# Performance work log

Measured on AMD Instinct MI355X. Metric: run time of the kernel, lower is better.

The kernel has to match this reference:

```python
import jax, jax.numpy as jnp
import numpy as np

# J2 (von Mises) plane-strain elastoplasticity with linear isotropic hardening
# (faithful stand-in for pyprnn's J2Material: elastic predictor + radial return,
#  committed history = plastic strain tensor + accumulated plastic strain).
E_MOD = 3130.0   # Young's modulus (epoxy, MPa)
NU = 0.37        # Poisson ratio
SIG_Y = 64.8     # initial yield stress
H_ISO = 300.0    # linear isotropic hardening modulus
MU = E_MOD / (2.0 * (1.0 + NU))
LAM = E_MOD * NU / ((1.0 + NU) * (1.0 - 2.0 * NU))


def j2_update(eps, eps_p, alpha):
    """eps: [P,3] (exx, eyy, gamma_xy engineering); eps_p: [P,4] (xx,yy,zz,xy tensorial);
    alpha: [P] accumulated plastic strain. Returns (stress [P,3], eps_p_new, alpha_new)."""
    ee_xx = eps[:, 0] - eps_p[:, 0]
    ee_yy = eps[:, 1] - eps_p[:, 1]
    ee_zz = -eps_p[:, 2]                      # plane strain: total ezz = 0
    ee_xy = 0.5 * eps[:, 2] - eps_p[:, 3]     # tensorial shear
    tr = ee_xx + ee_yy + ee_zz
    # trial (elastic predictor) stress
    sxx = LAM * tr + 2.0 * MU * ee_xx
    syy = LAM * tr + 2.0 * MU * ee_yy
    szz = LAM * tr + 2.0 * MU * ee_zz
    sxy = 2.0 * MU * ee_xy
    p = (sxx + syy + szz) / 3.0
    dxx, dyy, dzz = sxx - p, syy - p, szz - p
    q = jnp.sqrt(1.5 * (dxx * dxx + dyy * dyy + dzz * dzz + 2.0 * sxy * sxy))
    f = q - (SIG_Y + H_ISO * alpha)
    dgam = jnp.maximum(f, 0.0) / (3.0 * MU + H_ISO)   # radial return, closed form
    qs = jnp.maximum(q, 1e-12)
    nxx, nyy, nzz, nxy = 1.5 * dxx / qs, 1.5 * dyy / qs, 1.5 * dzz / qs, 1.5 * sxy / qs
    two_mu_dg = 2.0 * MU * dgam
    sig = jnp.stack([sxx - two_mu_dg * nxx, syy - two_mu_dg * nyy, sxy - two_mu_dg * nxy], axis=-1)
    eps_p_new = eps_p + dgam[:, None] * jnp.stack([nxx, nyy, nzz, nxy], axis=-1)
    alpha_new = alpha + dgam
    return sig, eps_p_new, alpha_new


def setup_inputs() -> dict:
    key = jax.random.key(0)
    k1, k2, k3 = jax.random.split(key, 3)
    B, T, F = 16384, 128, 3
    MATPTS = 16
    L, O = MATPTS * F, 3
    x = jax.random.normal(k1, (B, T, F), dtype=jnp.float32) * 0.02  # strain paths
    W1 = jax.random.normal(k2, (L, F), dtype=jnp.float32) * (1.0 / np.sqrt(F))
    W2 = jax.random.normal(k3, (O, L), dtype=jnp.float32) * (1.0 / np.sqrt(L))
    return {"x": x, "W1": W1, "W2": W2}


def reference(x, W1, W2):
    B, T, F = x.shape
    L = W1.shape[0]
    P = B * (L // F)                 # total material points = batch * mat_pts
    W2s = jax.nn.softplus(W2)        # SoftLayer: positive weights, no bias
    xt = jnp.swapaxes(x, 0, 1)       # [T, B, F]

    def step(carry, xi):
        eps_p, alpha = carry
        lat = xi @ W1.T                       # fc1 (no bias): [B, L]
        eps = lat.reshape(P, F)               # per-material-point strain
        sig, eps_p, alpha = j2_update(eps, eps_p, alpha)   # update + commit
        out = sig.reshape(B, L) @ W2s.T       # fc2 softplus-weighted linear
        return (eps_p, alpha), out

    carry0 = (jnp.zeros((P, 4), jnp.float32), jnp.zeros((P,), jnp.float32))
    _, ys = jax.lax.scan(step, carry0, xt)    # ys: [T, B, O]
    return jnp.swapaxes(ys, 0, 1)             # [B, T, O]
```

## Files before the change

### kernel.cpp

```cpp
#include <hip/hip_runtime.h>
#include <math.h>


#define BLOCK 256
#define BPB 16
#define TSTEPS 128
#define ROWF (TSTEPS * 3)
#define ROWP 388

#define DPP_REDUCE3(a, b, c)                                                          \
  asm volatile(                                                                       \
    "s_nop 1\n\t"                                                                     \
    "v_add_f32_dpp %0, %0, %0 row_shr:1 row_mask:0xf bank_mask:0xf bound_ctrl:1\n\t"  \
    "v_add_f32_dpp %1, %1, %1 row_shr:1 row_mask:0xf bank_mask:0xf bound_ctrl:1\n\t"  \
    "v_add_f32_dpp %2, %2, %2 row_shr:1 row_mask:0xf bank_mask:0xf bound_ctrl:1\n\t"  \
    "v_add_f32_dpp %0, %0, %0 row_shr:2 row_mask:0xf bank_mask:0xf bound_ctrl:1\n\t"  \
    "v_add_f32_dpp %1, %1, %1 row_shr:2 row_mask:0xf bank_mask:0xf bound_ctrl:1\n\t"  \
    "v_add_f32_dpp %2, %2, %2 row_shr:2 row_mask:0xf bank_mask:0xf bound_ctrl:1\n\t"  \
    "v_add_f32_dpp %0, %0, %0 row_shr:4 row_mask:0xf bank_mask:0xf bound_ctrl:1\n\t"  \
    "v_add_f32_dpp %1, %1, %1 row_shr:4 row_mask:0xf bank_mask:0xf bound_ctrl:1\n\t"  \
    "v_add_f32_dpp %2, %2, %2 row_shr:4 row_mask:0xf bank_mask:0xf bound_ctrl:1\n\t"  \
    "v_add_f32_dpp %0, %0, %0 row_shr:8 row_mask:0xf bank_mask:0xf bound_ctrl:1\n\t"  \
    "v_add_f32_dpp %1, %1, %1 row_shr:8 row_mask:0xf bank_mask:0xf bound_ctrl:1\n\t"  \
    "v_add_f32_dpp %2, %2, %2 row_shr:8 row_mask:0xf bank_mask:0xf bound_ctrl:1"      \
    : "+v"(a), "+v"(b), "+v"(c))

__global__ __launch_bounds__(BLOCK, 4)
void prnn_j2_kernel(const float* __restrict__ x,
                    const float* __restrict__ W1,
                    const float* __restrict__ W2,
                    float* __restrict__ out)
{
    constexpr float MU    = (float)(3130.0 / (2.0 * (1.0 + 0.37)));
    constexpr float LAM   = (float)(3130.0 * 0.37 / ((1.0 + 0.37) * (1.0 - 2.0 * 0.37)));
    constexpr float SIG_Y = 64.8f;
    constexpr float H_ISO = 300.0f;
    const float TWO_MU  = 2.0f * MU;
    const float K3MU    = 3.0f * MU;
    const float INV_DEN = 1.0f / (3.0f * MU + H_ISO);
    const float KBULK   = LAM + TWO_MU * (1.0f / 3.0f);
    const float C_Q2    = 6.0f * MU * MU;

    __shared__ float xs[BPB * ROWP + 12];

    const int tid = threadIdx.x;
    const int bl  = tid >> 4;
    const int m   = tid & 15;
    const bool m15 = (m == 15);
    const int blockBase = blockIdx.x * (BPB * ROWF);

    for (int i = tid; i < BPB * ROWF; i += BLOCK) {
        int b = i / ROWF;
        int r = i - b * ROWF;
        xs[b * ROWP + r] = x[blockBase + i];
    }

    float w1[3][3], w2s[3][3];
    #pragma unroll
    for (int c = 0; c < 3; ++c)
        #pragma unroll
        for (int f = 0; f < 3; ++f)
            w1[c][f] = W1[(3 * m + c) * 3 + f];
    #pragma unroll
    for (int o = 0; o < 3; ++o)
        #pragma unroll
        for (int c = 0; c < 3; ++c) {
            float w = W2[o * 48 + 3 * m + c];
            w2s[o][c] = fmaxf(w, 0.0f) + log1pf(expf(-fabsf(w)));
        }

    __syncthreads();

    float p0 = 0.f, p1 = 0.f, p2 = 0.f, p3 = 0.f;
    float yld = SIG_Y;
    float* xrow = &xs[bl * ROWP];
    float4* xv  = (float4*)xrow;

#define J2_STEP(x0_, x1_, x2_, wp_)                                          \
  {                                                                          \
    const float x0 = (x0_), x1 = (x1_), x2 = (x2_);                          \
    const float e0 = w1[0][0]*x0 + w1[0][1]*x1 + w1[0][2]*x2;                \
    const float e1 = w1[1][0]*x0 + w1[1][1]*x1 + w1[1][2]*x2;                \
    const float e2 = w1[2][0]*x0 + w1[2][1]*x1 + w1[2][2]*x2;                \
    const float ee_xx = e0 - p0;                                             \
    const float ee_yy = e1 - p1;                                             \
    const float ee_xy = fmaf(0.5f, e2, -p3);                                 \
    const float tr = (ee_xx + ee_yy) - p2;                                   \
    const float c3 = tr * (1.0f/3.0f);                                       \
    const float exd = ee_xx - c3;                                            \
    const float eyd = ee_yy - c3;                                            \
    const float ezd = -p2 - c3;                                              \
    float u = exd*exd; u = fmaf(eyd, eyd, u); u = fmaf(ezd, ezd, u);         \
    u = fmaf(ee_xy*ee_xy, 2.0f, u);                                          \
    const float q2 = fmaxf(C_Q2 * u, 1e-24f);                                \
    const float rq = __builtin_amdgcn_rsqf(q2);                              \
    const float q  = q2 * rq;                                                \
    const float dgam = fmaxf(q - yld, 0.0f) * INV_DEN;                       \
    yld = fmaf(H_ISO, dgam, yld);                                            \
    const float k   = K3MU * dgam * rq;                                      \
    const float omk = 1.0f - k;                                              \
    const float pm  = KBULK * tr;                                            \
    const float s0 = fmaf(TWO_MU*exd, omk, pm);                              \
    const float s1 = fmaf(TWO_MU*eyd, omk, pm);                              \
    const float s2 = (TWO_MU*ee_xy) * omk;                                   \
    p0 = fmaf(k, exd, p0);                                                   \
    p1 = fmaf(k, eyd, p1);                                                   \
    p2 = fmaf(k, ezd, p2);                                                   \
    p3 = fmaf(k, ee_xy, p3);                                                 \
    float o0 = w2s[0][0]*s0 + w2s[0][1]*s1 + w2s[0][2]*s2;                   \
    float o1 = w2s[1][0]*s0 + w2s[1][1]*s1 + w2s[1][2]*s2;                   \
    float o2 = w2s[2][0]*s0 + w2s[2][1]*s1 + w2s[2][2]*s2;                   \
    DPP_REDUCE3(o0, o1, o2);                                                 \
    if (m15) { (wp_)[0] = o0; (wp_)[1] = o1; (wp_)[2] = o2; }                \
  }

    float4 A = xv[0], Bv = xv[1], Cv = xv[2];
    for (int tb = 0; tb < TSTEPS / 4; ++tb) {
        float4 An = xv[3 * tb + 3];
        float4 Bn = xv[3 * tb + 4];
        float4 Cn = xv[3 * tb + 5];

        float* wp = xrow + 12 * tb;
        J2_STEP(A.x, A.y, A.z,  wp + 0);
        J2_STEP(A.w, Bv.x, Bv.y, wp + 3);
        J2_STEP(Bv.z, Bv.w, Cv.x, wp + 6);
        J2_STEP(Cv.y, Cv.z, Cv.w, wp + 9);

        A = An; Bv = Bn; Cv = Cn;
    }
#undef J2_STEP

    __syncthreads();

    for (int i = tid; i < BPB * ROWF; i += BLOCK) {
        int b = i / ROWF;
        int r = i - b * ROWF;
        out[blockBase + i] = xs[b * ROWP + r];
    }
}

extern "C" void kernel_launch(void* const* d_in, const int* in_sizes, int n_in,
                              void* d_out, int out_size, void* d_ws, size_t ws_size,
                              hipStream_t stream) {
    const float* x  = (const float*)d_in[0];
    const float* W1 = (const float*)d_in[1];
    const float* W2 = (const float*)d_in[2];
    float* out = (float*)d_out;

    const int B = 16384;
    dim3 grid(B / BPB);
    dim3 block(BLOCK);
    prnn_j2_kernel<<<grid, block, 0, stream>>>(x, W1, W2, out);
}
```

Before: 135.0 us.

## Pack two material points per thread with float2 math and 8-lane butterfly reduce

Each thread now handles two material points, using 2-wide vector types so the compiler can emit packed FP32 instructions. Each batch row then needs only 8 lanes, so a block covers 32 rows. The cross-lane sum becomes a 3-stage DPP butterfly over 8 lanes instead of a 4-stage shift reduction over 16. Global loads and stores are widened to float4. The trade-off is doubled per-thread state, shared memory and register pressure, with launch bounds lowered to 2 blocks per CU, and only 3 of every 8 lanes do the output writes.

```diff
diff --git a/kernel.cpp b/kernel.cpp
--- a/kernel.cpp
+++ b/kernel.cpp
@@ -3,29 +3,35 @@
 
 
 #define BLOCK 256
-#define BPB 16
+#define BPB 32
 #define TSTEPS 128
 #define ROWF (TSTEPS * 3)
 #define ROWP 388
 
-#define DPP_REDUCE3(a, b, c)                                                          \
-  asm volatile(                                                                       \
-    "s_nop 1\n\t"                                                                     \
-    "v_add_f32_dpp %0, %0, %0 row_shr:1 row_mask:0xf bank_mask:0xf bound_ctrl:1\n\t"  \
-    "v_add_f32_dpp %1, %1, %1 row_shr:1 row_mask:0xf bank_mask:0xf bound_ctrl:1\n\t"  \
-    "v_add_f32_dpp %2, %2, %2 row_shr:1 row_mask:0xf bank_mask:0xf bound_ctrl:1\n\t"  \
-    "v_add_f32_dpp %0, %0, %0 row_shr:2 row_mask:0xf bank_mask:0xf bound_ctrl:1\n\t"  \
-    "v_add_f32_dpp %1, %1, %1 row_shr:2 row_mask:0xf bank_mask:0xf bound_ctrl:1\n\t"  \
-    "v_add_f32_dpp %2, %2, %2 row_shr:2 row_mask:0xf bank_mask:0xf bound_ctrl:1\n\t"  \
-    "v_add_f32_dpp %0, %0, %0 row_shr:4 row_mask:0xf bank_mask:0xf bound_ctrl:1\n\t"  \
-    "v_add_f32_dpp %1, %1, %1 row_shr:4 row_mask:0xf bank_mask:0xf bound_ctrl:1\n\t"  \
-    "v_add_f32_dpp %2, %2, %2 row_shr:4 row_mask:0xf bank_mask:0xf bound_ctrl:1\n\t"  \
-    "v_add_f32_dpp %0, %0, %0 row_shr:8 row_mask:0xf bank_mask:0xf bound_ctrl:1\n\t"  \
-    "v_add_f32_dpp %1, %1, %1 row_shr:8 row_mask:0xf bank_mask:0xf bound_ctrl:1\n\t"  \
-    "v_add_f32_dpp %2, %2, %2 row_shr:8 row_mask:0xf bank_mask:0xf bound_ctrl:1"      \
+typedef float v2 __attribute__((ext_vector_type(2)));
+
+static __device__ __forceinline__ v2 vfma(v2 a, v2 b, v2 c) {
+    return __builtin_elementwise_fma(a, b, c);
+}
+static __device__ __forceinline__ v2 vmax(v2 a, v2 b) {
+    return __builtin_elementwise_max(a, b);
+}
+
+#define DPP_BFLY3(a, b, c)                                                       \
+  asm volatile(                                                                  \
+    "s_nop 1\n\t"                                                                \
+    "v_add_f32_dpp %0, %0, %0 quad_perm:[1,0,3,2] row_mask:0xf bank_mask:0xf\n\t"\
+    "v_add_f32_dpp %1, %1, %1 quad_perm:[1,0,3,2] row_mask:0xf bank_mask:0xf\n\t"\
+    "v_add_f32_dpp %2, %2, %2 quad_perm:[1,0,3,2] row_mask:0xf bank_mask:0xf\n\t"\
+    "v_add_f32_dpp %0, %0, %0 quad_perm:[2,3,0,1] row_mask:0xf bank_mask:0xf\n\t"\
+    "v_add_f32_dpp %1, %1, %1 quad_perm:[2,3,0,1] row_mask:0xf bank_mask:0xf\n\t"\
+    "v_add_f32_dpp %2, %2, %2 quad_perm:[2,3,0,1] row_mask:0xf bank_mask:0xf\n\t"\
+    "v_add_f32_dpp %0, %0, %0 row_half_mirror row_mask:0xf bank_mask:0xf\n\t"    \
+    "v_add_f32_dpp %1, %1, %1 row_half_mirror row_mask:0xf bank_mask:0xf\n\t"    \
+    "v_add_f32_dpp %2, %2, %2 row_half_mirror row_mask:0xf bank_mask:0xf"        \
     : "+v"(a), "+v"(b), "+v"(c))
 
-__global__ __launch_bounds__(BLOCK, 4)
+__global__ __launch_bounds__(BLOCK, 2)
 void prnn_j2_kernel(const float* __restrict__ x,
                     const float* __restrict__ W1,
                     const float* __restrict__ W2,
@@ -40,78 +46,97 @@
     const float INV_DEN = 1.0f / (3.0f * MU + H_ISO);
     const float KBULK   = LAM + TWO_MU * (1.0f / 3.0f);
     const float C_Q2    = 6.0f * MU * MU;
+    const v2 VTHIRD = {1.0f/3.0f, 1.0f/3.0f};
+    const v2 VQMIN  = {1e-24f, 1e-24f};
+    const v2 VZERO  = {0.0f, 0.0f};
 
     __shared__ float xs[BPB * ROWP + 12];
 
     const int tid = threadIdx.x;
-    const int bl  = tid >> 4;
-    const int m   = tid & 15;
-    const bool m15 = (m == 15);
+    const int bl  = tid >> 3;
+    const int l   = tid & 7;
     const int blockBase = blockIdx.x * (BPB * ROWF);
 
-    for (int i = tid; i < BPB * ROWF; i += BLOCK) {
-        int b = i / ROWF;
-        int r = i - b * ROWF;
-        xs[b * ROWP + r] = x[blockBase + i];
+    {
+        const float4* xg = (const float4*)(x + blockBase);
+        for (int i4 = tid; i4 < BPB * ROWF / 4; i4 += BLOCK) {
+            int b  = i4 / (ROWF / 4);
+            int r4 = i4 - b * (ROWF / 4);
+            ((float4*)(xs + b * ROWP))[r4] = xg[i4];
+        }
     }
 
-    float w1[3][3], w2s[3][3];
+    const int pa = l, pb = l + 8;
+    v2 w1p[3][3], w2p[3][3];
     #pragma unroll
     for (int c = 0; c < 3; ++c)
         #pragma unroll
-        for (int f = 0; f < 3; ++f)
-            w1[c][f] = W1[(3 * m + c) * 3 + f];
+        for (int f = 0; f < 3; ++f) {
+            w1p[c][f].x = W1[(3 * pa + c) * 3 + f];
+            w1p[c][f].y = W1[(3 * pb + c) * 3 + f];
+        }
     #pragma unroll
     for (int o = 0; o < 3; ++o)
         #pragma unroll
         for (int c = 0; c < 3; ++c) {
-            float w = W2[o * 48 + 3 * m + c];
-            w2s[o][c] = fmaxf(w, 0.0f) + log1pf(expf(-fabsf(w)));
+            float wa = W2[o * 48 + 3 * pa + c];
+            float wb = W2[o * 48 + 3 * pb + c];
+            w2p[o][c].x = fmaxf(wa, 0.0f) + log1pf(expf(-fabsf(wa)));
+            w2p[o][c].y = fmaxf(wb, 0.0f) + log1pf(expf(-fabsf(wb)));
         }
 
     __syncthreads();
 
-    float p0 = 0.f, p1 = 0.f, p2 = 0.f, p3 = 0.f;
-    float yld = SIG_Y;
+    v2 p0 = VZERO, p1 = VZERO, p2 = VZERO, p3 = VZERO;
+    v2 yld = {SIG_Y, SIG_Y};
     float* xrow = &xs[bl * ROWP];
-    float4* xv  = (float4*)xrow;
+    const float4* xv = (const float4*)xrow;
 
 #define J2_STEP(x0_, x1_, x2_, wp_)                                          \
   {                                                                          \
-    const float x0 = (x0_), x1 = (x1_), x2 = (x2_);                          \
-    const float e0 = w1[0][0]*x0 + w1[0][1]*x1 + w1[0][2]*x2;                \
-    const float e1 = w1[1][0]*x0 + w1[1][1]*x1 + w1[1][2]*x2;                \
-    const float e2 = w1[2][0]*x0 + w1[2][1]*x1 + w1[2][2]*x2;                \
-    const float ee_xx = e0 - p0;                                             \
-    const float ee_yy = e1 - p1;                                             \
-    const float ee_xy = fmaf(0.5f, e2, -p3);                                 \
-    const float tr = (ee_xx + ee_yy) - p2;                                   \
-    const float c3 = tr * (1.0f/3.0f);                                       \
-    const float exd = ee_xx - c3;                                            \
-    const float eyd = ee_yy - c3;                                            \
-    const float ezd = -p2 - c3;                                              \
-    float u = exd*exd; u = fmaf(eyd, eyd, u); u = fmaf(ezd, ezd, u);         \
-    u = fmaf(ee_xy*ee_xy, 2.0f, u);                                          \
-    const float q2 = fmaxf(C_Q2 * u, 1e-24f);                                \
-    const float rq = __builtin_amdgcn_rsqf(q2);                              \
-    const float q  = q2 * rq;                                                \
-    const float dgam = fmaxf(q - yld, 0.0f) * INV_DEN;                       \
-    yld = fmaf(H_ISO, dgam, yld);                                            \
-    const float k   = K3MU * dgam * rq;                                      \
-    const float omk = 1.0f - k;                                              \
-    const float pm  = KBULK * tr;                                            \
-    const float s0 = fmaf(TWO_MU*exd, omk, pm);                              \
-    const float s1 = fmaf(TWO_MU*eyd, omk, pm);                              \
-    const float s2 = (TWO_MU*ee_xy) * omk;                                   \
-    p0 = fmaf(k, exd, p0);                                                   \
-    p1 = fmaf(k, eyd, p1);                                                   \
-    p2 = fmaf(k, ezd, p2);                                                   \
-    p3 = fmaf(k, ee_xy, p3);                                                 \
-    float o0 = w2s[0][0]*s0 + w2s[0][1]*s1 + w2s[0][2]*s2;                   \
-    float o1 = w2s[1][0]*s0 + w2s[1][1]*s1 + w2s[1][2]*s2;                   \
-    float o2 = w2s[2][0]*s0 + w2s[2][1]*s1 + w2s[2][2]*s2;                   \
-    DPP_REDUCE3(o0, o1, o2);                                                 \
-    if (m15) { (wp_)[0] = o0; (wp_)[1] = o1; (wp_)[2] = o2; }                \
+    const float x0s = (x0_), x1s = (x1_), x2s = (x2_);                       \
+    const v2 x0 = {x0s, x0s}, x1 = {x1s, x1s}, x2 = {x2s, x2s};              \
+    const v2 e0 = vfma(w1p[0][0], x0, vfma(w1p[0][1], x1, w1p[0][2] * x2));  \
+    const v2 e1 = vfma(w1p[1][0], x0, vfma(w1p[1][1], x1, w1p[1][2] * x2));  \
+    const v2 e2 = vfma(w1p[2][0], x0, vfma(w1p[2][1], x1, w1p[2][2] * x2));  \
+    const v2 ee_xx = e0 - p0;                                                \
+    const v2 ee_yy = e1 - p1;                                                \
+    const v2 ee_xy = 0.5f * e2 - p3;                                         \
+    const v2 tr = (ee_xx + ee_yy) - p2;                                      \
+    const v2 c3 = tr * VTHIRD;                                               \
+    const v2 exd = ee_xx - c3;                                               \
+    const v2 eyd = ee_yy - c3;                                               \
+    const v2 ezd = -p2 - c3;                                                 \
+    v2 u = exd * exd;                                                        \
+    u = vfma(eyd, eyd, u);                                                   \
+    u = vfma(ezd, ezd, u);                                                   \
+    const v2 t2 = ee_xy * ee_xy;                                             \
+    u = vfma(t2, (v2){2.0f, 2.0f}, u);                                       \
+    const v2 q2 = vmax(C_Q2 * u, VQMIN);                                     \
+    v2 rq;                                                                   \
+    rq.x = __builtin_amdgcn_rsqf(q2.x);                                      \
+    rq.y = __builtin_amdgcn_rsqf(q2.y);                                      \
+    const v2 q = q2 * rq;                                                    \
+    const v2 dgam = vmax(q - yld, VZERO) * INV_DEN;                          \
+    yld = vfma((v2){H_ISO, H_ISO}, dgam, yld);                               \
+    const v2 k   = (K3MU * dgam) * rq;                                       \
+    const v2 omk = 1.0f - k;                                                 \
+    const v2 pm  = KBULK * tr;                                               \
+    const v2 s0 = vfma(TWO_MU * exd, omk, pm);                               \
+    const v2 s1 = vfma(TWO_MU * eyd, omk, pm);                               \
+    const v2 s2 = (TWO_MU * ee_xy) * omk;                                    \
+    p0 = vfma(k, exd, p0);                                                   \
+    p1 = vfma(k, eyd, p1);                                                   \
+    p2 = vfma(k, ezd, p2);                                                   \
+    p3 = vfma(k, ee_xy, p3);                                                 \
+    v2 q0 = vfma(w2p[0][0], s0, vfma(w2p[0][1], s1, w2p[0][2] * s2));        \
+    v2 q1 = vfma(w2p[1][0], s0, vfma(w2p[1][1], s1, w2p[1][2] * s2));        \
+    v2 q2o = vfma(w2p[2][0], s0, vfma(w2p[2][1], s1, w2p[2][2] * s2));       \
+    float o0 = q0.x + q0.y;                                                  \
+    float o1 = q1.x + q1.y;                                                  \
+    float o2 = q2o.x + q2o.y;                                                \
+    DPP_BFLY3(o0, o1, o2);                                                   \
+    if (l < 3) { (wp_)[l] = (l == 0) ? o0 : ((l == 1) ? o1 : o2); }          \
   }
 
     float4 A = xv[0], Bv = xv[1], Cv = xv[2];
@@ -121,8 +146,8 @@
         float4 Cn = xv[3 * tb + 5];
 
         float* wp = xrow + 12 * tb;
-        J2_STEP(A.x, A.y, A.z,  wp + 0);
-        J2_STEP(A.w, Bv.x, Bv.y, wp + 3);
+        J2_STEP(A.x,  A.y,  A.z,  wp + 0);
+        J2_STEP(A.w,  Bv.x, Bv.y, wp + 3);
         J2_STEP(Bv.z, Bv.w, Cv.x, wp + 6);
         J2_STEP(Cv.y, Cv.z, Cv.w, wp + 9);
 
@@ -132,10 +157,13 @@
 
     __syncthreads();
 
-    for (int i = tid; i < BPB * ROWF; i += BLOCK) {
-        int b = i / ROWF;
-        int r = i - b * ROWF;
-        out[blockBase + i] = xs[b * ROWP + r];
+    {
+        float4* og = (float4*)(out + blockBase);
+        for (int i4 = tid; i4 < BPB * ROWF / 4; i4 += BLOCK) {
+            int b  = i4 / (ROWF / 4);
+            int r4 = i4 - b * (ROWF / 4);
+            og[i4] = ((const float4*)(xs + b * ROWP))[r4];
+        }
     }
 }
 
```

Result: faster. 123.0 us (-8.9%).
